# Performance work log

Measured on AMD Instinct MI355X. Metric: run time of the kernel, lower is better.

## Reference

```python
import jax, jax.numpy as jnp
import numpy as np

N, IN_F, OUT_F = 4096, 512, 16
HID = [128, 64, 32]
H = 4  # num_head
LRELU_SLOPE = 0.2
BN_EPS = 1e-5
NEG_INF = -1e9


def _gat(x, adj_mask, W, a_src, a_dst, heads, f_out):
    n = x.shape[0]
    h = (x @ W).reshape(n, heads, f_out)              # [N,H,F]
    es = jnp.einsum('nhf,hf->hn', h, a_src)           # [H,N]
    ed = jnp.einsum('nhf,hf->hn', h, a_dst)           # [H,N]
    e = jax.nn.leaky_relu(es[:, :, None] + ed[:, None, :], LRELU_SLOPE)  # [H,N,N]
    e = jnp.where(adj_mask[None], e, NEG_INF)
    attn = jax.nn.softmax(e, axis=-1)                 # masked softmax over neighbors
    out = jnp.einsum('hij,jhf->ihf', attn, h)         # [N,H,F]
    return out.reshape(n, heads * f_out)


def _bn_elu(x, gamma, beta):
    mu = jnp.mean(x, axis=0)
    var = jnp.var(x, axis=0)
    xhat = (x - mu) * jax.lax.rsqrt(var + BN_EPS)
    return jax.nn.elu(xhat * gamma + beta)


def setup_inputs() -> dict:
    key = jax.random.key(0)
    ks = jax.random.split(key, 14)
    s = lambda fin: 1.0 / np.sqrt(fin)
    x = jax.random.normal(ks[0], (N, IN_F), jnp.float32)
    adj = jax.random.randint(ks[1], (N, N), 0, 2, jnp.int32)
    W1 = jax.random.normal(ks[2], (IN_F, H * HID[0]), jnp.float32) * s(IN_F)
    a1s = jax.random.normal(ks[3], (H, HID[0]), jnp.float32) * s(HID[0])
    a1d = jax.random.normal(ks[4], (H, HID[0]), jnp.float32) * s(HID[0])
    lw1 = jax.random.normal(ks[5], (H * HID[0], HID[1]), jnp.float32) * s(H * HID[0])
    lb1 = jnp.zeros((HID[1],), jnp.float32)
    g1 = jnp.ones((HID[1],), jnp.float32)
    be1 = jnp.zeros((HID[1],), jnp.float32)
    W2 = jax.random.normal(ks[6], (HID[1], H * HID[2]), jnp.float32) * s(HID[1])
    a2s = jax.random.normal(ks[7], (H, HID[2]), jnp.float32) * s(HID[2])
    a2d = jax.random.normal(ks[8], (H, HID[2]), jnp.float32) * s(HID[2])
    lw2 = jax.random.normal(ks[9], (H * HID[2], OUT_F), jnp.float32) * s(H * HID[2])
    lb2 = jnp.zeros((OUT_F,), jnp.float32)
    g2 = jnp.ones((OUT_F,), jnp.float32)
    be2 = jnp.zeros((OUT_F,), jnp.float32)
    return dict(x=x, adj=adj, W1=W1, a1s=a1s, a1d=a1d, lw1=lw1, lb1=lb1, g1=g1, be1=be1,
                W2=W2, a2s=a2s, a2d=a2d, lw2=lw2, lb2=lb2, g2=g2, be2=be2)


def reference(x, adj, W1, a1s, a1d, lw1, lb1, g1, be1, W2, a2s, a2d, lw2, lb2, g2, be2):
    adj_mask = adj > 0
    x1 = _gat(x, adj_mask, W1, a1s, a1d, H, HID[0])        # [N, H*128]
    x2 = _bn_elu(x1 @ lw1 + lb1, g1, be1)                  # [N, 64]
    x3 = _gat(x2, adj_mask, W2, a2s, a2d, H, HID[2])       # [N, H*32]
    out = _bn_elu(x3 @ lw2 + lb2, g2, be2)                 # [N, 16]
    return out
```

## Files before the change

kernel.cpp:

```cpp
#include <hip/hip_runtime.h>
#include <hip/hip_bf16.h>
#include <stdint.h>

#define NN 4096
#define H4 4

typedef __hip_bfloat16 bf16;
typedef unsigned short ushort_t;
typedef unsigned long long ull_t;
typedef __attribute__((ext_vector_type(4))) float f32x4;
typedef __attribute__((ext_vector_type(8))) short s16x8;

__device__ __forceinline__ ushort_t f2bf(float f) {
  unsigned u = __float_as_uint(f);
  return (ushort_t)((u + 0x7fff + ((u >> 16) & 1)) >> 16);
}
__device__ __forceinline__ float bf2f(ushort_t h) {
  return __uint_as_float((unsigned)h << 16);
}
__device__ __forceinline__ short2 pkbf(float a, float b) {
  union { __hip_bfloat162 h; short2 s; } u;
  u.h = __float22bfloat162_rn(make_float2(a, b));
  return u.s;
}
__device__ __forceinline__ s16x8 as_s16x8(uint4 v) {
  union { uint4 u; s16x8 s; } c; c.u = v; return c.s;
}

__global__ __launch_bounds__(256) void k_mask(const int* __restrict__ adj,
                                              ull_t* __restrict__ mask) {
  int row = blockIdx.x, tid = threadIdx.x;
  int lane = tid & 63, wv = tid >> 6;
  const int* arow = adj + (size_t)row * NN;
  for (int c = 0; c < NN; c += 256) {
    int col = c + wv * 64 + lane;
    ull_t b = __ballot(arow[col] != 0);
    if (lane == 0) mask[row * 64 + (c >> 6) + wv] = b;
  }
}

__global__ __launch_bounds__(256) void k_gemm(const float* __restrict__ A,
                                              const float* __restrict__ B,
                                              const float* __restrict__ bias,
                                              float* __restrict__ C, int M, int K, int Nc) {
  __shared__ float As[16][68];
  __shared__ float Bs[16][68];
  int tid = threadIdx.x;
  int tx = tid & 15, ty = tid >> 4;
  int mBase = blockIdx.y * 64, nBase = blockIdx.x * 64;
  float acc[4][4] = {};
  for (int k0 = 0; k0 < K; k0 += 16) {
#pragma unroll
    for (int l = 0; l < 4; ++l) {
      int idx = l * 256 + tid;
      int m = idx >> 4, k = idx & 15;
      As[k][m] = A[(size_t)(mBase + m) * K + (k0 + k)];
    }
#pragma unroll
    for (int l = 0; l < 4; ++l) {
      int idx = l * 256 + tid;
      int k = idx >> 6, n = idx & 63;
      int gn = nBase + n;
      Bs[k][n] = (gn < Nc) ? B[(size_t)(k0 + k) * Nc + gn] : 0.f;
    }
    __syncthreads();
#pragma unroll
    for (int k = 0; k < 16; ++k) {
      float4 a = *(const float4*)&As[k][ty * 4];
      float4 b = *(const float4*)&Bs[k][tx * 4];
      float av[4] = {a.x, a.y, a.z, a.w};
      float bv[4] = {b.x, b.y, b.z, b.w};
#pragma unroll
      for (int r = 0; r < 4; ++r)
#pragma unroll
        for (int c = 0; c < 4; ++c) acc[r][c] += av[r] * bv[c];
    }
    __syncthreads();
  }
#pragma unroll
  for (int r = 0; r < 4; ++r) {
    int gm = mBase + ty * 4 + r;
#pragma unroll
    for (int c = 0; c < 4; ++c) {
      int gn = nBase + tx * 4 + c;
      if (gn < Nc) {
        float v = acc[r][c];
        if (bias) v += bias[gn];
        C[(size_t)gm * Nc + gn] = v;
      }
    }
  }
}

#define APLANE (4096 * 512)
template <int KK, int NC>
__device__ __forceinline__ void packW_dev(const float* __restrict__ W,
                                          ushort_t* __restrict__ pk, int tau, int lane) {
  constexpr int KS = KK / 32;
  constexpr int T = (NC / 16) * KS;
  constexpr int PL = T * 512;
  if (tau >= T) return;
  int q = lane >> 4, nn = lane & 15;
  int ct = tau / KS, ks = tau % KS;
  ushort_t hi[8], lo[8];
#pragma unroll
  for (int u = 0; u < 8; ++u) {
    float v = W[(size_t)(ks * 32 + q * 8 + u) * NC + ct * 16 + nn];
    hi[u] = f2bf(v);
    lo[u] = f2bf(v - bf2f(hi[u]));
  }
  size_t idx = ((size_t)(ct * KS + ks) * 64 + lane) * 8;
  *(uint4*)&pk[idx] = *(uint4*)hi;
  *(uint4*)&pk[PL + idx] = *(uint4*)lo;
}

__global__ __launch_bounds__(256) void k_packP(const float* __restrict__ x,
                                               const float* __restrict__ W1,
                                               const float* __restrict__ lw1,
                                               const float* __restrict__ lw2,
                                               ushort_t* __restrict__ pkA,
                                               ushort_t* __restrict__ pkW1,
                                               ushort_t* __restrict__ pkLW1,
                                               ushort_t* __restrict__ pkLW2) {
  int b = blockIdx.x, t = threadIdx.x;
  int w = t >> 6, lane = t & 63;
  if (b < 1024) {
    int q = lane >> 4, nn = lane & 15;
    int tau = b * 4 + w;
    int mt = tau >> 4, ks = tau & 15;
    const float* src = &x[(size_t)(mt * 16 + nn) * 512 + ks * 32 + q * 8];
    float4 v0 = *(const float4*)src;
    float4 v1 = *(const float4*)(src + 4);
    float vv[8] = {v0.x, v0.y, v0.z, v0.w, v1.x, v1.y, v1.z, v1.w};
    ushort_t hi[8], lo[8];
#pragma unroll
    for (int u = 0; u < 8; ++u) {
      hi[u] = f2bf(vv[u]);
      lo[u] = f2bf(vv[u] - bf2f(hi[u]));
    }
    size_t idx = ((size_t)(mt * 16 + ks) * 64 + lane) * 8;
    *(uint4*)&pkA[idx] = *(uint4*)hi;
    *(uint4*)&pkA[APLANE + idx] = *(uint4*)lo;
  } else if (b < 1152) {
    packW_dev<512, 512>(W1, pkW1, (b - 1024) * 4 + w, lane);
  } else if (b < 1168) {
    packW_dev<512, 64>(lw1, pkLW1, (b - 1152) * 4 + w, lane);
  } else {
    packW_dev<128, 16>(lw2, pkLW2, (b - 1168) * 4 + w, lane);
  }
}

__global__ __launch_bounds__(256, 1) void k_mm1(const uint4* __restrict__ pkA,
                                                const uint4* __restrict__ pkW,
                                                float* __restrict__ h1) {
  constexpr int APL4 = APLANE / 8;
  constexpr int WPL4 = (512 / 16) * (512 / 32) * 64;
  int t = threadIdx.x;
  int w = t >> 6, lane = t & 63;
  int q = lane >> 4, nn = lane & 15;
  int mt0 = blockIdx.x * 4 + (w & 1) * 2;
  int ct0 = blockIdx.y * 8 + (w >> 1) * 4;
  f32x4 acc[2][4];
#pragma unroll
  for (int rt = 0; rt < 2; ++rt)
#pragma unroll
    for (int c = 0; c < 4; ++c)
#pragma unroll
      for (int k = 0; k < 4; ++k) acc[rt][c][k] = 0.f;
#pragma unroll
  for (int ks = 0; ks < 16; ++ks) {
    int ia0 = (mt0 * 16 + ks) * 64 + lane;
    int ia1 = ((mt0 + 1) * 16 + ks) * 64 + lane;
    uint4 ah0 = pkA[ia0], ah1 = pkA[ia1];
    uint4 al0 = pkA[APL4 + ia0], al1 = pkA[APL4 + ia1];
    uint4 bh[4], bl[4];
#pragma unroll
    for (int c = 0; c < 4; ++c) {
      int ib = ((ct0 + c) * 16 + ks) * 64 + lane;
      bh[c] = pkW[ib];
      bl[c] = pkW[WPL4 + ib];
    }
#pragma unroll
    for (int c = 0; c < 4; ++c) {
      acc[0][c] = __builtin_amdgcn_mfma_f32_16x16x32_bf16(as_s16x8(ah0), as_s16x8(bh[c]), acc[0][c], 0, 0, 0);
      acc[0][c] = __builtin_amdgcn_mfma_f32_16x16x32_bf16(as_s16x8(ah0), as_s16x8(bl[c]), acc[0][c], 0, 0, 0);
      acc[0][c] = __builtin_amdgcn_mfma_f32_16x16x32_bf16(as_s16x8(al0), as_s16x8(bh[c]), acc[0][c], 0, 0, 0);
      acc[1][c] = __builtin_amdgcn_mfma_f32_16x16x32_bf16(as_s16x8(ah1), as_s16x8(bh[c]), acc[1][c], 0, 0, 0);
      acc[1][c] = __builtin_amdgcn_mfma_f32_16x16x32_bf16(as_s16x8(ah1), as_s16x8(bl[c]), acc[1][c], 0, 0, 0);
      acc[1][c] = __builtin_amdgcn_mfma_f32_16x16x32_bf16(as_s16x8(al1), as_s16x8(bh[c]), acc[1][c], 0, 0, 0);
    }
  }
  int rowB = blockIdx.x * 64 + (w & 1) * 32;
#pragma unroll
  for (int rt = 0; rt < 2; ++rt)
#pragma unroll
    for (int c = 0; c < 4; ++c)
#pragma unroll
      for (int reg = 0; reg < 4; ++reg) {
        int gi = rowB + rt * 16 + q * 4 + reg;
        h1[(size_t)gi * 512 + (ct0 + c) * 16 + nn] = acc[rt][c][reg];
      }
}

template <int F, int TB>
__global__ __launch_bounds__(TB) void k_pack(const float* __restrict__ h,
                                             ushort_t* __restrict__ pk) {
  constexpr int CTW = TB / 64;
  int t = threadIdx.x;
  int lane = t & 63, ctw = t >> 6;
  int q = lane >> 4, nn = lane & 15;
  int ks = blockIdx.x, hd = blockIdx.y;
#pragma unroll
  for (int ct = ctw; ct < F / 16; ct += CTW) {
    ushort_t v[8];
#pragma unroll
    for (int u = 0; u < 8; ++u)
      v[u] = f2bf(h[(size_t)(ks * 32 + q * 8 + u) * (H4 * F) + hd * F + ct * 16 + nn]);
    *(uint4*)&pk[((((size_t)hd * (F / 16) + ct) * (NN / 32) + ks) * 64 + lane) * 8] =
        *(uint4*)v;
  }
}

template <int F>
__global__ __launch_bounds__(256) void k_scores(const float* __restrict__ h,
                                                const float* __restrict__ a_s,
                                                const float* __restrict__ a_d,
                                                float* __restrict__ Tt, float* __restrict__ E1,
                                                float* __restrict__ E2, float* __restrict__ D1,
                                                float* __restrict__ D2) {
  int idx = blockIdx.x * 256 + threadIdx.x;
  if (idx >= NN * H4) return;
  int n = idx >> 2, hd = idx & 3;
  const float* hp = h + (size_t)n * (H4 * F) + hd * F;
  const float* sp = a_s + hd * F;
  const float* dp = a_d + hd * F;
  float ss = 0.f, sd = 0.f;
#pragma unroll 4
  for (int f = 0; f < F; ++f) {
    float v = hp[f];
    ss += v * sp[f];
    sd += v * dp[f];
  }
  ss = fminf(fmaxf(ss, -30.f), 30.f);
  sd = fminf(fmaxf(sd, -30.f), 30.f);
  int o = hd * NN + n;
  Tt[o] = __expf(-ss);
  E1[o] = __expf(ss);
  E2[o] = __expf(0.2f * ss);
  D1[o] = __expf(sd);
  D2[o] = __expf(0.2f * sd);
}

__device__ __forceinline__ s16x8 build_af(float E1i, float E2i, float Ti, unsigned byt,
                                          float4 d1a, float4 d1b, float4 d2a, float4 d2b,
                                          float& rs) {
  float d1[8] = {d1a.x, d1a.y, d1a.z, d1a.w, d1b.x, d1b.y, d1b.z, d1b.w};
  float d2[8] = {d2a.x, d2a.y, d2a.z, d2a.w, d2b.x, d2b.y, d2b.z, d2b.w};
  union { s16x8 v; short2 p[4]; } A;
#pragma unroll
  for (int tp = 0; tp < 4; ++tp) {
    int k0 = 2 * tp, k1 = 2 * tp + 1;
    bool p0 = d1[k0] > Ti;
    float u0 = (p0 ? E1i : E2i) * (p0 ? d1[k0] : d2[k0]);
    u0 = (byt & (1u << k0)) ? u0 : 0.f;
    bool p1 = d1[k1] > Ti;
    float u1 = (p1 ? E1i : E2i) * (p1 ? d1[k1] : d2[k1]);
    u1 = (byt & (1u << k1)) ? u1 : 0.f;
    rs += u0 + u1;
    A.p[tp] = pkbf(u0, u1);
  }
  return A.v;
}

template <int F, int OUTM>
__global__ __launch_bounds__(256, 4) void k_agg_mfma(
    const uint4* __restrict__ pk, const float* __restrict__ Tt,
    const float* __restrict__ E1, const float* __restrict__ E2,
    const float* __restrict__ D1, const float* __restrict__ D2,
    const ull_t* __restrict__ mask, ushort_t* __restrict__ pkOut) {
  constexpr int CT = F / 16;
  constexpr int KSO = (H4 * F) / 32;
  constexpr int OPL = NN * H4 * F;
  __shared__ float red[2 * 16 * F];
  __shared__ float rsred[16 * 4];
  int t = threadIdx.x;
  int w = t >> 6, lane = t & 63;
  int q = lane >> 4, nn = lane & 15;
  int hd = blockIdx.y;
  int rowBase = blockIdx.x * 16;
  int jBase = w * (NN / 4);
  int ia = rowBase + nn;
  float E1i = E1[hd * NN + ia];
  float E2i = E2[hd * NN + ia];
  float Ti = Tt[hd * NN + ia];
  const ull_t* mkp = mask + (size_t)ia * 64;
  const float* d1h = D1 + hd * NN;
  const float* d2h = D2 + hd * NN;

  f32x4 acc[CT];
#pragma unroll
  for (int cc = 0; cc < CT; ++cc)
#pragma unroll
    for (int k = 0; k < 4; ++k) acc[cc][k] = 0.f;
  float rs = 0.f;

  for (int jc = 0; jc < NN / 4 / 64; ++jc) {
    int j0 = jBase + jc * 64;
    int ks0 = j0 >> 5;
    ull_t mk = mkp[j0 >> 6];
    float4 d1a = *(const float4*)&d1h[j0 + q * 8];
    float4 d1b = *(const float4*)&d1h[j0 + q * 8 + 4];
    float4 d2a = *(const float4*)&d2h[j0 + q * 8];
    float4 d2b = *(const float4*)&d2h[j0 + q * 8 + 4];
    float4 d1c = *(const float4*)&d1h[j0 + 32 + q * 8];
    float4 d1d = *(const float4*)&d1h[j0 + 32 + q * 8 + 4];
    float4 d2c = *(const float4*)&d2h[j0 + 32 + q * 8];
    float4 d2d = *(const float4*)&d2h[j0 + 32 + q * 8 + 4];
    s16x8 a0 = build_af(E1i, E2i, Ti, (unsigned)(mk >> (q * 8)) & 0xffu, d1a, d1b, d2a, d2b, rs);
    s16x8 a1 = build_af(E1i, E2i, Ti, (unsigned)(mk >> (32 + q * 8)) & 0xffu, d1c, d1d, d2c, d2d, rs);
    uint4 bv[CT];
#pragma unroll
    for (int cc = 0; cc < CT; ++cc)
      bv[cc] = pk[(size_t)((hd * CT + cc) * (NN / 32) + ks0) * 64 + lane];
#pragma unroll
    for (int cc = 0; cc < CT; ++cc)
      acc[cc] = __builtin_amdgcn_mfma_f32_16x16x32_bf16(a0, as_s16x8(bv[cc]), acc[cc], 0, 0, 0);
#pragma unroll
    for (int cc = 0; cc < CT; ++cc)
      bv[cc] = pk[(size_t)((hd * CT + cc) * (NN / 32) + ks0 + 1) * 64 + lane];
#pragma unroll
    for (int cc = 0; cc < CT; ++cc)
      acc[cc] = __builtin_amdgcn_mfma_f32_16x16x32_bf16(a1, as_s16x8(bv[cc]), acc[cc], 0, 0, 0);
  }

  rs += __shfl_xor(rs, 16, 64);
  rs += __shfl_xor(rs, 32, 64);
  if (q == 0) rsred[nn * 4 + w] = rs;

#define IDX(cc, reg) (((q * 4 + reg) * F) + cc * 16 + nn)
  if (w == 1) {
#pragma unroll
    for (int cc = 0; cc < CT; ++cc)
#pragma unroll
      for (int reg = 0; reg < 4; ++reg) red[IDX(cc, reg)] = acc[cc][reg];
  }
  if (w == 3) {
#pragma unroll
    for (int cc = 0; cc < CT; ++cc)
#pragma unroll
      for (int reg = 0; reg < 4; ++reg) red[16 * F + IDX(cc, reg)] = acc[cc][reg];
  }
  __syncthreads();
  if (w == 0) {
#pragma unroll
    for (int cc = 0; cc < CT; ++cc)
#pragma unroll
      for (int reg = 0; reg < 4; ++reg) acc[cc][reg] += red[IDX(cc, reg)];
  }
  if (w == 2) {
#pragma unroll
    for (int cc = 0; cc < CT; ++cc)
#pragma unroll
      for (int reg = 0; reg < 4; ++reg) {
        acc[cc][reg] += red[16 * F + IDX(cc, reg)];
        red[16 * F + IDX(cc, reg)] = acc[cc][reg];
      }
  }
  __syncthreads();
  if (w == 0) {
    float rinv[4];
#pragma unroll
    for (int reg = 0; reg < 4; ++reg) {
      float4 rv = *(float4*)&rsred[(q * 4 + reg) * 4];
      float s = (rv.x + rv.y) + (rv.z + rv.w);
      rinv[reg] = (s > 0.f) ? 1.f / s : 0.f;
    }
#pragma unroll
    for (int cc = 0; cc < CT; ++cc)
#pragma unroll
      for (int reg = 0; reg < 4; ++reg) {
        float v = (acc[cc][reg] + red[16 * F + IDX(cc, reg)]) * rinv[reg];
        int gi = rowBase + q * 4 + reg;
        int c = hd * F + cc * 16 + nn;
        int mt = gi >> 4, rowin = gi & 15;
        int ks = c >> 5, qp = (c >> 3) & 3, u = c & 7;
        size_t idx = (((size_t)mt * KSO + ks) * 64 + qp * 16 + rowin) * 8 + u;
        ushort_t hi = f2bf(v);
        pkOut[idx] = hi;
        if (OUTM == 1) pkOut[OPL + idx] = f2bf(v - bf2f(hi));
      }
  }
#undef IDX
}

__global__ __launch_bounds__(256) void k_mm2(const uint4* __restrict__ pkX,
                                             const uint4* __restrict__ pkW,
                                             const float* __restrict__ bias,
                                             float* __restrict__ y) {
  constexpr int WPL4 = 4 * 16 * 64;
  __shared__ float red[2 * 16 * 64];
  int t = threadIdx.x;
  int w = t >> 6, lane = t & 63;
  int q = lane >> 4, nn = lane & 15;
  int mt = blockIdx.x * 2 + (w & 1);
  int kh = w >> 1;
  f32x4 acc[4];
#pragma unroll
  for (int c = 0; c < 4; ++c)
#pragma unroll
    for (int k = 0; k < 4; ++k) acc[c][k] = 0.f;
#pragma unroll
  for (int k8 = 0; k8 < 8; ++k8) {
    int ks = kh * 8 + k8;
    uint4 a = pkX[(mt * 16 + ks) * 64 + lane];
#pragma unroll
    for (int c = 0; c < 4; ++c) {
      uint4 bh = pkW[(c * 16 + ks) * 64 + lane];
      uint4 bl = pkW[WPL4 + (c * 16 + ks) * 64 + lane];
      acc[c] = __builtin_amdgcn_mfma_f32_16x16x32_bf16(as_s16x8(a), as_s16x8(bh), acc[c], 0, 0, 0);
      acc[c] = __builtin_amdgcn_mfma_f32_16x16x32_bf16(as_s16x8(a), as_s16x8(bl), acc[c], 0, 0, 0);
    }
  }
  int base = (w & 1) * 1024;
  if (kh == 1) {
#pragma unroll
    for (int c = 0; c < 4; ++c)
#pragma unroll
      for (int reg = 0; reg < 4; ++reg)
        red[base + (q * 4 + reg) * 64 + c * 16 + nn] = acc[c][reg];
  }
  __syncthreads();
  if (kh == 0) {
#pragma unroll
    for (int c = 0; c < 4; ++c)
#pragma unroll
      for (int reg = 0; reg < 4; ++reg) {
        float v = acc[c][reg] + red[base + (q * 4 + reg) * 64 + c * 16 + nn] + bias[c * 16 + nn];
        y[(size_t)(mt * 16 + q * 4 + reg) * 64 + c * 16 + nn] = v;
      }
  }
}

__global__ __launch_bounds__(256) void k_mm4(const uint4* __restrict__ pkX,
                                             const uint4* __restrict__ pkW,
                                             const float* __restrict__ bias,
                                             float* __restrict__ y) {
  constexpr int XPL4 = 256 * 4 * 64;
  constexpr int WPL4 = 1 * 4 * 64;
  int t = threadIdx.x;
  int w = t >> 6, lane = t & 63;
  int q = lane >> 4, nn = lane & 15;
  int mt = blockIdx.x * 4 + w;
  f32x4 acc;
#pragma unroll
  for (int k = 0; k < 4; ++k) acc[k] = 0.f;
#pragma unroll
  for (int ks = 0; ks < 4; ++ks) {
    uint4 ah = pkX[(mt * 4 + ks) * 64 + lane];
    uint4 al = pkX[XPL4 + (mt * 4 + ks) * 64 + lane];
    uint4 bh = pkW[ks * 64 + lane];
    uint4 bl = pkW[WPL4 + ks * 64 + lane];
    acc = __builtin_amdgcn_mfma_f32_16x16x32_bf16(as_s16x8(ah), as_s16x8(bh), acc, 0, 0, 0);
    acc = __builtin_amdgcn_mfma_f32_16x16x32_bf16(as_s16x8(ah), as_s16x8(bl), acc, 0, 0, 0);
    acc = __builtin_amdgcn_mfma_f32_16x16x32_bf16(as_s16x8(al), as_s16x8(bh), acc, 0, 0, 0);
  }
  float b = bias[nn];
#pragma unroll
  for (int reg = 0; reg < 4; ++reg)
    y[(size_t)(mt * 16 + q * 4 + reg) * 16 + nn] = acc[reg] + b;
}

__global__ __launch_bounds__(256) void k_bn_col(const float* __restrict__ y,
                                                const float* __restrict__ gamma,
                                                const float* __restrict__ beta,
                                                float* __restrict__ o, int C) {
  int c = blockIdx.x, tid = threadIdx.x;
  float s = 0.f, s2 = 0.f;
  for (int r = tid; r < NN; r += 256) {
    float v = y[(size_t)r * C + c];
    s += v;
    s2 += v * v;
  }
  __shared__ float sh[256], sh2[256];
  __shared__ float smu, srs;
  sh[tid] = s; sh2[tid] = s2;
  __syncthreads();
  for (int off = 128; off; off >>= 1) {
    if (tid < off) { sh[tid] += sh[tid + off]; sh2[tid] += sh2[tid + off]; }
    __syncthreads();
  }
  if (tid == 0) {
    float mu = sh[0] * (1.f / NN);
    float var = sh2[0] * (1.f / NN) - mu * mu;
    smu = mu;
    srs = rsqrtf(fmaxf(var, 0.f) + 1e-5f);
  }
  __syncthreads();
  float mu = smu, rstd = srs, g = gamma[c], b = beta[c];
  for (int r = tid; r < NN; r += 256) {
    float v = (y[(size_t)r * C + c] - mu) * rstd * g + b;
    v = v > 0.f ? v : (__expf(v) - 1.f);
    o[(size_t)r * C + c] = v;
  }
}

extern "C" void kernel_launch(void* const* d_in, const int* in_sizes, int n_in,
                              void* d_out, int out_size, void* d_ws, size_t ws_size,
                              hipStream_t stream) {
  (void)in_sizes; (void)n_in; (void)out_size; (void)ws_size;
  const float* x   = (const float*)d_in[0];
  const int*   adj = (const int*)d_in[1];
  const float* W1  = (const float*)d_in[2];
  const float* a1s = (const float*)d_in[3];
  const float* a1d = (const float*)d_in[4];
  const float* lw1 = (const float*)d_in[5];
  const float* lb1 = (const float*)d_in[6];
  const float* g1  = (const float*)d_in[7];
  const float* be1 = (const float*)d_in[8];
  const float* W2  = (const float*)d_in[9];
  const float* a2s = (const float*)d_in[10];
  const float* a2d = (const float*)d_in[11];
  const float* lw2 = (const float*)d_in[12];
  const float* lb2 = (const float*)d_in[13];
  const float* g2  = (const float*)d_in[14];
  const float* be2 = (const float*)d_in[15];
  float* out = (float*)d_out;

  char* w = (char*)d_ws;
  const size_t MB = 1u << 20;
  ull_t*    mask  = (ull_t*)(w + 0);
  ushort_t* pkA   = (ushort_t*)(w + 2 * MB);
  ushort_t* pkW1  = (ushort_t*)(w + 10 * MB);
  float*    h1    = (float*)(w + 11 * MB);
  ushort_t* pk1   = (ushort_t*)(w + 19 * MB);
  float*    T1    = (float*)(w + 23 * MB);
  float*    E1a   = T1 + 16384;
  float*    E2a   = E1a + 16384;
  float*    D1a   = E2a + 16384;
  float*    D2a   = D1a + 16384;
  ushort_t* pkX1  = (ushort_t*)(w + 24 * MB);
  ushort_t* pkLW1 = (ushort_t*)(w + 28 * MB);
  float*    y1    = (float*)(w + 29 * MB);
  float*    x2    = (float*)(w + 30 * MB);
  float*    h2    = (float*)(w + 31 * MB);
  ushort_t* pk2   = (ushort_t*)(w + 33 * MB);
  float*    T2    = (float*)(w + 34 * MB);
  float*    E1b   = T2 + 16384;
  float*    E2b   = E1b + 16384;
  float*    D1b   = E2b + 16384;
  float*    D2b   = D1b + 16384;
  ushort_t* pkX3  = (ushort_t*)(w + 35 * MB);
  ushort_t* pkLW2 = (ushort_t*)(w + 37 * MB);
  float*    y2    = (float*)(w + 37 * MB + 131072);

  k_mask<<<NN, 256, 0, stream>>>(adj, mask);
  k_packP<<<1169, 256, 0, stream>>>(x, W1, lw1, lw2, pkA, pkW1, pkLW1, pkLW2);

  k_mm1<<<dim3(64, 4), 256, 0, stream>>>((const uint4*)pkA, (const uint4*)pkW1, h1);
  k_pack<128, 256><<<dim3(NN / 32, H4), 256, 0, stream>>>(h1, pk1);
  k_scores<128><<<(NN * H4) / 256, 256, 0, stream>>>(h1, a1s, a1d, T1, E1a, E2a, D1a, D2a);
  k_agg_mfma<128, 0><<<dim3(NN / 16, H4), 256, 0, stream>>>((const uint4*)pk1, T1, E1a, E2a,
                                                            D1a, D2a, mask, pkX1);

  k_mm2<<<128, 256, 0, stream>>>((const uint4*)pkX1, (const uint4*)pkLW1, lb1, y1);
  k_bn_col<<<64, 256, 0, stream>>>(y1, g1, be1, x2, 64);

  k_gemm<<<dim3(2, 64), 256, 0, stream>>>(x2, W2, nullptr, h2, NN, 64, 128);
  k_pack<32, 128><<<dim3(NN / 32, H4), 128, 0, stream>>>(h2, pk2);
  k_scores<32><<<(NN * H4) / 256, 256, 0, stream>>>(h2, a2s, a2d, T2, E1b, E2b, D1b, D2b);
  k_agg_mfma<32, 1><<<dim3(NN / 16, H4), 256, 0, stream>>>((const uint4*)pk2, T2, E1b, E2b,
                                                           D1b, D2b, mask, pkX3);

  k_mm4<<<64, 256, 0, stream>>>((const uint4*)pkX3, (const uint4*)pkLW2, lb2, y2);
  k_bn_col<<<16, 256, 0, stream>>>(y2, g2, be2, out, 16);
}
```

Baseline: 329.4 us.

## Process two row tiles per block in GAT aggregation to reuse B fragments

Each aggregation block now handles 32 destination rows (two 16-row MFMA tiles) instead of 16. The packed feature (B) fragments and the D1/D2 score loads are fetched once and shared by both tiles, halving global traffic for h per output row. The accumulator and LDS reduction buffers double, and launch bounds drop from 4 to 2 waves per SIMD to make room for the extra registers, which lowers occupancy. The grid is halved to match.

```diff
diff --git a/kernel.cpp b/kernel.cpp
--- a/kernel.cpp
+++ b/kernel.cpp
@@ -273,7 +273,7 @@
 }
 
 template <int F, int OUTM>
-__global__ __launch_bounds__(256, 4) void k_agg_mfma(
+__global__ __launch_bounds__(256, 2) void k_agg_mfma(
     const uint4* __restrict__ pk, const float* __restrict__ Tt,
     const float* __restrict__ E1, const float* __restrict__ E2,
     const float* __restrict__ D1, const float* __restrict__ D2,
@@ -281,33 +281,41 @@
   constexpr int CT = F / 16;
   constexpr int KSO = (H4 * F) / 32;
   constexpr int OPL = NN * H4 * F;
-  __shared__ float red[2 * 16 * F];
-  __shared__ float rsred[16 * 4];
+  __shared__ float red[2 * 32 * F];
+  __shared__ float rsred[32 * 4];
   int t = threadIdx.x;
   int w = t >> 6, lane = t & 63;
   int q = lane >> 4, nn = lane & 15;
   int hd = blockIdx.y;
-  int rowBase = blockIdx.x * 16;
+  int rowBase = blockIdx.x * 32;
   int jBase = w * (NN / 4);
-  int ia = rowBase + nn;
-  float E1i = E1[hd * NN + ia];
-  float E2i = E2[hd * NN + ia];
-  float Ti = Tt[hd * NN + ia];
-  const ull_t* mkp = mask + (size_t)ia * 64;
+  int ia0 = rowBase + nn, ia1 = rowBase + 16 + nn;
+  float E1i0 = E1[hd * NN + ia0], E2i0 = E2[hd * NN + ia0], Ti0 = Tt[hd * NN + ia0];
+  float E1i1 = E1[hd * NN + ia1], E2i1 = E2[hd * NN + ia1], Ti1 = Tt[hd * NN + ia1];
+  const ull_t* mk0p = mask + (size_t)ia0 * 64;
+  const ull_t* mk1p = mask + (size_t)ia1 * 64;
   const float* d1h = D1 + hd * NN;
   const float* d2h = D2 + hd * NN;
 
-  f32x4 acc[CT];
-#pragma unroll
-  for (int cc = 0; cc < CT; ++cc)
-#pragma unroll
-    for (int k = 0; k < 4; ++k) acc[cc][k] = 0.f;
-  float rs = 0.f;
+  f32x4 acc[2][CT];
+#pragma unroll
+  for (int rt = 0; rt < 2; ++rt)
+#pragma unroll
+    for (int cc = 0; cc < CT; ++cc)
+#pragma unroll
+      for (int k = 0; k < 4; ++k) acc[rt][cc][k] = 0.f;
+  float rs0 = 0.f, rs1 = 0.f;
 
   for (int jc = 0; jc < NN / 4 / 64; ++jc) {
     int j0 = jBase + jc * 64;
     int ks0 = j0 >> 5;
-    ull_t mk = mkp[j0 >> 6];
+    uint4 bv[2][CT];
+#pragma unroll
+    for (int s = 0; s < 2; ++s)
+#pragma unroll
+      for (int cc = 0; cc < CT; ++cc)
+        bv[s][cc] = pk[(size_t)((hd * CT + cc) * (NN / 32) + ks0 + s) * 64 + lane];
+    ull_t mk0 = mk0p[j0 >> 6], mk1 = mk1p[j0 >> 6];
     float4 d1a = *(const float4*)&d1h[j0 + q * 8];
     float4 d1b = *(const float4*)&d1h[j0 + q * 8 + 4];
     float4 d2a = *(const float4*)&d2h[j0 + q * 8];
@@ -316,79 +324,87 @@
     float4 d1d = *(const float4*)&d1h[j0 + 32 + q * 8 + 4];
     float4 d2c = *(const float4*)&d2h[j0 + 32 + q * 8];
     float4 d2d = *(const float4*)&d2h[j0 + 32 + q * 8 + 4];
-    s16x8 a0 = build_af(E1i, E2i, Ti, (unsigned)(mk >> (q * 8)) & 0xffu, d1a, d1b, d2a, d2b, rs);
-    s16x8 a1 = build_af(E1i, E2i, Ti, (unsigned)(mk >> (32 + q * 8)) & 0xffu, d1c, d1d, d2c, d2d, rs);
-    uint4 bv[CT];
+    s16x8 a00 = build_af(E1i0, E2i0, Ti0, (unsigned)(mk0 >> (q * 8)) & 0xffu, d1a, d1b, d2a, d2b, rs0);
+    s16x8 a01 = build_af(E1i0, E2i0, Ti0, (unsigned)(mk0 >> (32 + q * 8)) & 0xffu, d1c, d1d, d2c, d2d, rs0);
+    s16x8 a10 = build_af(E1i1, E2i1, Ti1, (unsigned)(mk1 >> (q * 8)) & 0xffu, d1a, d1b, d2a, d2b, rs1);
+    s16x8 a11 = build_af(E1i1, E2i1, Ti1, (unsigned)(mk1 >> (32 + q * 8)) & 0xffu, d1c, d1d, d2c, d2d, rs1);
 #pragma unroll
     for (int cc = 0; cc < CT; ++cc)
-      bv[cc] = pk[(size_t)((hd * CT + cc) * (NN / 32) + ks0) * 64 + lane];
+      acc[0][cc] = __builtin_amdgcn_mfma_f32_16x16x32_bf16(a00, as_s16x8(bv[0][cc]), acc[0][cc], 0, 0, 0);
 #pragma unroll
     for (int cc = 0; cc < CT; ++cc)
-      acc[cc] = __builtin_amdgcn_mfma_f32_16x16x32_bf16(a0, as_s16x8(bv[cc]), acc[cc], 0, 0, 0);
+      acc[0][cc] = __builtin_amdgcn_mfma_f32_16x16x32_bf16(a01, as_s16x8(bv[1][cc]), acc[0][cc], 0, 0, 0);
 #pragma unroll
     for (int cc = 0; cc < CT; ++cc)
-      bv[cc] = pk[(size_t)((hd * CT + cc) * (NN / 32) + ks0 + 1) * 64 + lane];
+      acc[1][cc] = __builtin_amdgcn_mfma_f32_16x16x32_bf16(a10, as_s16x8(bv[0][cc]), acc[1][cc], 0, 0, 0);
 #pragma unroll
     for (int cc = 0; cc < CT; ++cc)
-      acc[cc] = __builtin_amdgcn_mfma_f32_16x16x32_bf16(a1, as_s16x8(bv[cc]), acc[cc], 0, 0, 0);
-  }
-
-  rs += __shfl_xor(rs, 16, 64);
-  rs += __shfl_xor(rs, 32, 64);
-  if (q == 0) rsred[nn * 4 + w] = rs;
-
-#define IDX(cc, reg) (((q * 4 + reg) * F) + cc * 16 + nn)
-  if (w == 1) {
-#pragma unroll
-    for (int cc = 0; cc < CT; ++cc)
-#pragma unroll
-      for (int reg = 0; reg < 4; ++reg) red[IDX(cc, reg)] = acc[cc][reg];
-  }
-  if (w == 3) {
-#pragma unroll
-    for (int cc = 0; cc < CT; ++cc)
-#pragma unroll
-      for (int reg = 0; reg < 4; ++reg) red[16 * F + IDX(cc, reg)] = acc[cc][reg];
+      acc[1][cc] = __builtin_amdgcn_mfma_f32_16x16x32_bf16(a11, as_s16x8(bv[1][cc]), acc[1][cc], 0, 0, 0);
+  }
+
+  rs0 += __shfl_xor(rs0, 16, 64); rs0 += __shfl_xor(rs0, 32, 64);
+  rs1 += __shfl_xor(rs1, 16, 64); rs1 += __shfl_xor(rs1, 32, 64);
+  if (q == 0) {
+    rsred[nn * 4 + w] = rs0;
+    rsred[(16 + nn) * 4 + w] = rs1;
+  }
+
+#define IDX(rt, cc, reg) ((rt * 16 + q * 4 + reg) * F + cc * 16 + nn)
+  if (w == 1 || w == 3) {
+    int base = (w >> 1) * 32 * F;
+#pragma unroll
+    for (int rt = 0; rt < 2; ++rt)
+#pragma unroll
+      for (int cc = 0; cc < CT; ++cc)
+#pragma unroll
+        for (int reg = 0; reg < 4; ++reg) red[base + IDX(rt, cc, reg)] = acc[rt][cc][reg];
+  }
+  __syncthreads();
+  if (w == 0 || w == 2) {
+    int base = (w >> 1) * 32 * F;
+#pragma unroll
+    for (int rt = 0; rt < 2; ++rt)
+#pragma unroll
+      for (int cc = 0; cc < CT; ++cc)
+#pragma unroll
+        for (int reg = 0; reg < 4; ++reg) acc[rt][cc][reg] += red[base + IDX(rt, cc, reg)];
+  }
+  if (w == 2) {
+#pragma unroll
+    for (int rt = 0; rt < 2; ++rt)
+#pragma unroll
+      for (int cc = 0; cc < CT; ++cc)
+#pragma unroll
+        for (int reg = 0; reg < 4; ++reg) red[32 * F + IDX(rt, cc, reg)] = acc[rt][cc][reg];
   }
   __syncthreads();
   if (w == 0) {
-#pragma unroll
-    for (int cc = 0; cc < CT; ++cc)
-#pragma unroll
-      for (int reg = 0; reg < 4; ++reg) acc[cc][reg] += red[IDX(cc, reg)];
-  }
-  if (w == 2) {
-#pragma unroll
-    for (int cc = 0; cc < CT; ++cc)
+    float rinv[2][4];
+#pragma unroll
+    for (int rt = 0; rt < 2; ++rt)
 #pragma unroll
       for (int reg = 0; reg < 4; ++reg) {
-        acc[cc][reg] += red[16 * F + IDX(cc, reg)];
-        red[16 * F + IDX(cc, reg)] = acc[cc][reg];
+        int row = rt * 16 + q * 4 + reg;
+        float4 rv = *(float4*)&rsred[row * 4];
+        float s = (rv.x + rv.y) + (rv.z + rv.w);
+        rinv[rt][reg] = (s > 0.f) ? 1.f / s : 0.f;
       }
-  }
-  __syncthreads();
-  if (w == 0) {
-    float rinv[4];
-#pragma unroll
-    for (int reg = 0; reg < 4; ++reg) {
-      float4 rv = *(float4*)&rsred[(q * 4 + reg) * 4];
-      float s = (rv.x + rv.y) + (rv.z + rv.w);
-      rinv[reg] = (s > 0.f) ? 1.f / s : 0.f;
-    }
-#pragma unroll
-    for (int cc = 0; cc < CT; ++cc)
-#pragma unroll
-      for (int reg = 0; reg < 4; ++reg) {
-        float v = (acc[cc][reg] + red[16 * F + IDX(cc, reg)]) * rinv[reg];
-        int gi = rowBase + q * 4 + reg;
-        int c = hd * F + cc * 16 + nn;
-        int mt = gi >> 4, rowin = gi & 15;
-        int ks = c >> 5, qp = (c >> 3) & 3, u = c & 7;
-        size_t idx = (((size_t)mt * KSO + ks) * 64 + qp * 16 + rowin) * 8 + u;
-        ushort_t hi = f2bf(v);
-        pkOut[idx] = hi;
-        if (OUTM == 1) pkOut[OPL + idx] = f2bf(v - bf2f(hi));
-      }
+#pragma unroll
+    for (int rt = 0; rt < 2; ++rt)
+#pragma unroll
+      for (int cc = 0; cc < CT; ++cc)
+#pragma unroll
+        for (int reg = 0; reg < 4; ++reg) {
+          float v = (acc[rt][cc][reg] + red[32 * F + IDX(rt, cc, reg)]) * rinv[rt][reg];
+          int gi = rowBase + rt * 16 + q * 4 + reg;
+          int c = hd * F + cc * 16 + nn;
+          int mt = gi >> 4, rowin = gi & 15;
+          int ks = c >> 5, qp = (c >> 3) & 3, u = c & 7;
+          size_t idx = (((size_t)mt * KSO + ks) * 64 + qp * 16 + rowin) * 8 + u;
+          ushort_t hi = f2bf(v);
+          pkOut[idx] = hi;
+          if (OUTM == 1) pkOut[OPL + idx] = f2bf(v - bf2f(hi));
+        }
   }
 #undef IDX
 }
@@ -559,7 +575,7 @@
   k_mm1<<<dim3(64, 4), 256, 0, stream>>>((const uint4*)pkA, (const uint4*)pkW1, h1);
   k_pack<128, 256><<<dim3(NN / 32, H4), 256, 0, stream>>>(h1, pk1);
   k_scores<128><<<(NN * H4) / 256, 256, 0, stream>>>(h1, a1s, a1d, T1, E1a, E2a, D1a, D2a);
-  k_agg_mfma<128, 0><<<dim3(NN / 16, H4), 256, 0, stream>>>((const uint4*)pk1, T1, E1a, E2a,
+  k_agg_mfma<128, 0><<<dim3(NN / 32, H4), 256, 0, stream>>>((const uint4*)pk1, T1, E1a, E2a,
                                                             D1a, D2a, mask, pkX1);
 
   k_mm2<<<128, 256, 0, stream>>>((const uint4*)pkX1, (const uint4*)pkLW1, lb1, y1);
@@ -568,7 +584,7 @@
   k_gemm<<<dim3(2, 64), 256, 0, stream>>>(x2, W2, nullptr, h2, NN, 64, 128);
   k_pack<32, 128><<<dim3(NN / 32, H4), 128, 0, stream>>>(h2, pk2);
   k_scores<32><<<(NN * H4) / 256, 256, 0, stream>>>(h2, a2s, a2d, T2, E1b, E2b, D1b, D2b);
-  k_agg_mfma<32, 1><<<dim3(NN / 16, H4), 256, 0, stream>>>((const uint4*)pk2, T2, E1b, E2b,
+  k_agg_mfma<32, 1><<<dim3(NN / 32, H4), 256, 0, stream>>>((const uint4*)pk2, T2, E1b, E2b,
                                                            D1b, D2b, mask, pkX3);
 
   k_mm4<<<64, 256, 0, stream>>>((const uint4*)pkX3, (const uint4*)pkLW2, lb2, y2);
```

New measurement: 294.0 us, median of 2. 10.8% less time.
